# Optimization experiments

Hardware: AMD Instinct MI355X
Metric: run time of the kernel (lower is better)

Reference implementation:

```python
import jax, jax.numpy as jnp
import numpy as np

_DIR_INLIER = 0.9          # _HOUGHVOTING_DIRECTION_INLIER
_NUM_INLIER = 500          # _HOUGHVOTING_NUM_INLIER
_LABEL_THRESH = 500        # _LABEL2MASK_THRESHOL
NUM_CLASSES = 10
BS, H, W = 1, 240, 320


def setup_inputs() -> dict:
    key = jax.random.key(0)
    k_lab, k_cx, k_cy, k_nx, k_ny, k_nd = jax.random.split(key, 6)
    label = jax.random.randint(k_lab, (BS, H, W), 0, NUM_CLASSES + 1).astype(jnp.int32)
    xs = jnp.arange(W, dtype=jnp.float32)
    ys = jnp.arange(H, dtype=jnp.float32)
    xv, yv = jnp.meshgrid(xs, ys)  # [H, W] each
    # per-class ground-truth centers well inside the image so voting converges
    cxs = jax.random.uniform(k_cx, (NUM_CLASSES,), minval=40.0, maxval=W - 40.0)
    cys = jax.random.uniform(k_cy, (NUM_CLASSES,), minval=40.0, maxval=H - 40.0)
    dx = cxs[:, None, None] - xv[None]  # [C, H, W]
    dy = cys[:, None, None] - yv[None]
    nrm = jnp.sqrt(dx * dx + dy * dy) + 1e-6
    dirx = dx / nrm + 0.01 * jax.random.normal(k_nx, (NUM_CLASSES, H, W))
    diry = dy / nrm + 0.01 * jax.random.normal(k_ny, (NUM_CLASSES, H, W))
    depth = (1.0 + 0.3 * jnp.arange(NUM_CLASSES, dtype=jnp.float32))[:, None, None] \
        + 0.01 * jax.random.normal(k_nd, (NUM_CLASSES, H, W))
    cmap = jnp.stack([dirx, diry, depth], axis=1).reshape(3 * NUM_CLASSES, H, W)
    centermap = jnp.broadcast_to(cmap[None], (BS, 3 * NUM_CLASSES, H, W)).astype(jnp.float32)
    return {"label": label, "centermap": centermap}


def hough_voting(label, centermap, num_classes):
    bs, H_, W_ = label.shape
    xs = jnp.arange(W_, dtype=jnp.float32)
    ys = jnp.arange(H_, dtype=jnp.float32)
    xv, yv = jnp.meshgrid(xs, ys)            # [H, W]
    xsi = jnp.arange(W_, dtype=jnp.int32)
    all_centers, all_depths = [], []
    for b in range(bs):
        lab = label[b]
        row_c, row_d = [], []
        for cls in range(1, num_classes + 1):
            cmask = lab == cls                                    # [H, W]
            enough = cmask.sum() >= _LABEL_THRESH
            c3 = centermap[b, (cls - 1) * 3:(cls - 1) * 3 + 3]    # [3, H, W]
            slope = c3[1] / c3[0]                                  # dy/dx per pixel
            # every masked pixel votes along its line at every column x
            y_idx = jnp.round(yv[:, :, None] + slope[:, :, None] * (xs[None, None, :] - xv[:, :, None])).astype(jnp.int32)  # [H, W, W]
            valid = (y_idx >= 0) & (y_idx < H_) & cmask[:, :, None]
            bins = jnp.clip(y_idx, 0, H_ - 1) * W_ + xsi[None, None, :]
            hist = jnp.zeros(H_ * W_, jnp.float32).at[bins.ravel()].add(valid.ravel().astype(jnp.float32))
            cbin = jnp.argmax(hist)
            inlier_num = hist[cbin]
            cx = (cbin % W_).astype(jnp.float32)
            cy = (cbin // W_).astype(jnp.float32)
            # depth: mean of depth channel over direction-consistent class pixels
            disx = xv - cx
            disy = yv - cy
            dnrm = jnp.sqrt(disx * disx + disy * disy)
            dot = jnp.abs((disx / dnrm) * c3[0] + (disy / dnrm) * c3[1])  # nan at center -> compares False, as torch
            imask = (dot >= _DIR_INLIER) & cmask
            cnt = imask.sum().astype(jnp.float32)
            dsum = jnp.sum(jnp.where(imask, c3[2], 0.0))
            dmean = jnp.where(cnt > 0, dsum / jnp.maximum(cnt, 1.0), jnp.nan)
            trig = enough & (inlier_num > _NUM_INLIER)
            row_c.append(jnp.where(trig, jnp.stack([cx, cy]), jnp.zeros(2, jnp.float32)))
            row_d.append(jnp.where(trig, dmean, 0.0))
        all_centers.append(jnp.stack(row_c))
        all_depths.append(jnp.stack(row_d))
    return jnp.stack(all_centers), jnp.stack(all_depths)


def reference(label, centermap):
    return hough_voting(label, centermap, NUM_CLASSES)
```

## Files before the change

kernel.cpp:

```cpp
#include <hip/hip_runtime.h>
#include <stdint.h>

#define H 240
#define W 320
#define NPIX (H * W)
#define NCLS 10
#define TILE 16
#define HPAD 241
#define BIN_BITS 20
#define BIN_MASK 0xFFFFFu


__global__ void k_init(uint32_t* ws) {
    int i = threadIdx.x;
    if (i < 128) ws[i] = 0;
}

__global__ __launch_bounds__(256) void k_compact(const int* __restrict__ label,
                                                 const float* __restrict__ cm,
                                                 uint32_t* __restrict__ cls_cnt,
                                                 uint2* __restrict__ list) {
    __shared__ uint32_t lcnt[NCLS];
    __shared__ uint32_t lbase[NCLS];
    int p = blockIdx.x * 256 + threadIdx.x;
    if (threadIdx.x < NCLS) lcnt[threadIdx.x] = 0;
    __syncthreads();

    int l = label[p];
    bool match = (l >= 1 && l <= NCLS);
    int cls = l - 1;
    uint32_t li = 0;
    if (match) li = atomicAdd(&lcnt[cls], 1u);
    __syncthreads();

    if (threadIdx.x < NCLS) {
        uint32_t c = lcnt[threadIdx.x];
        lbase[threadIdx.x] = c ? atomicAdd(&cls_cnt[threadIdx.x], c) : 0u;
    }
    __syncthreads();

    if (match) {
        float dirx = cm[(cls * 3 + 0) * NPIX + p];
        float diry = cm[(cls * 3 + 1) * NPIX + p];
        float slope = diry / dirx;
        int y = p / W, x = p - y * W;
        uint2 e;
        e.x = (uint32_t)(x | (y << 16));
        e.y = __float_as_uint(slope);
        list[cls * NPIX + lbase[cls] + li] = e;
    }
}

__global__ __launch_bounds__(1024) void k_vote(const uint32_t* __restrict__ cls_cnt,
                                               const uint2* __restrict__ list,
                                               unsigned long long* __restrict__ best) {
    int cls = blockIdx.y;
    int x0 = blockIdx.x * TILE;
    __shared__ uint32_t hist[TILE * HPAD];
    __shared__ unsigned long long wred[16];
    int tid = threadIdx.x;
    for (int i = tid; i < TILE * HPAD; i += 1024) hist[i] = 0;
    __syncthreads();

    int n = (int)cls_cnt[cls];
    const uint2* lst = list + cls * NPIX;
    int wave = tid >> 6, lane = tid & 63;
    int g = lane >> 4, cit = lane & 15;
    float colf = (float)(x0 + cit);
    uint32_t* hcol = &hist[cit * HPAD];
    for (int i = wave * 4 + g; i < n; i += 64) {
        uint2 e = lst[i];
        float slope = __uint_as_float(e.y);
        float xf = (float)(e.x & 0xFFFFu);
        float yf = (float)(e.x >> 16);
        float r = rintf(yf + slope * (colf - xf));
        if (r >= 0.0f && r <= 239.0f) atomicAdd(&hcol[(int)r], 1u);
    }
    __syncthreads();

    unsigned long long k = 0;
    for (int i = tid; i < TILE * H; i += 1024) {
        int c = i / H, y = i - c * H;
        uint32_t v = hist[c * HPAD + y];
        uint32_t bin = (uint32_t)(y * W + x0 + c);
        unsigned long long key =
            ((unsigned long long)v << BIN_BITS) | (unsigned long long)(BIN_MASK - bin);
        if (key > k) k = key;
    }
#pragma unroll
    for (int off = 32; off > 0; off >>= 1) {
        unsigned long long o = __shfl_down(k, off);
        if (o > k) k = o;
    }
    if (lane == 0) wred[wave] = k;
    __syncthreads();
    if (tid == 0) {
        unsigned long long kk = wred[0];
#pragma unroll
        for (int w = 1; w < 16; ++w) if (wred[w] > kk) kk = wred[w];
        atomicMax(&best[cls], kk);
    }
}

__global__ __launch_bounds__(256) void k_inlier_final(
    const int* __restrict__ label, const float* __restrict__ cm,
    const uint32_t* __restrict__ cls_cnt,
    const unsigned long long* __restrict__ best,
    uint32_t* __restrict__ icnt, float* __restrict__ dsum,
    uint32_t* __restrict__ done, float* __restrict__ out) {
    __shared__ float scx[NCLS], scy[NCLS];
    __shared__ uint32_t scnt[NCLS];
    __shared__ float ssum[NCLS];
    __shared__ int slast;
    int tid = threadIdx.x;
    if (tid < NCLS) {
        unsigned long long key = best[tid];
        uint32_t bin = BIN_MASK - (uint32_t)(key & BIN_MASK);
        scx[tid] = (float)(bin % W);
        scy[tid] = (float)(bin / W);
        scnt[tid] = 0u;
        ssum[tid] = 0.0f;
    }
    __syncthreads();

    int p = blockIdx.x * 256 + tid;
    int l = label[p];
    if (l >= 1 && l <= NCLS) {
        int cls = l - 1;
        int y = p / W, x = p - y * W;
        float disx = (float)x - scx[cls];
        float disy = (float)y - scy[cls];
        float dn = sqrtf(disx * disx + disy * disy);
        if (dn > 0.0f) {
            float c0 = cm[(cls * 3 + 0) * NPIX + p];
            float c1 = cm[(cls * 3 + 1) * NPIX + p];
            float dot = fabsf((disx / dn) * c0 + (disy / dn) * c1);
            if (dot >= 0.9f) {
                atomicAdd(&scnt[cls], 1u);
                atomicAdd(&ssum[cls], cm[(cls * 3 + 2) * NPIX + p]);
            }
        }
    }
    __syncthreads();

    if (tid < NCLS) {
        if (scnt[tid]) atomicAdd(&icnt[tid], scnt[tid]);
        if (ssum[tid] != 0.0f) atomicAdd(&dsum[tid], ssum[tid]);
    }
    if (tid == 0) {
        __threadfence();
        uint32_t d = atomicAdd(done, 1u);
        slast = (d == (uint32_t)(gridDim.x - 1)) ? 1 : 0;
    }
    __syncthreads();

    if (slast && tid < NCLS) {
        uint32_t tc = atomicAdd(&icnt[tid], 0u);
        float td = atomicAdd(&dsum[tid], 0.0f);
        unsigned long long key = best[tid];
        uint32_t hv = (uint32_t)(key >> BIN_BITS);
        bool trig = (cls_cnt[tid] >= 500u) && (hv > 500u);
        float c = (float)tc;
        float dm = (c > 0.0f) ? (td / fmaxf(c, 1.0f)) : __builtin_nanf("");
        out[tid * 2 + 0] = trig ? scx[tid] : 0.0f;
        out[tid * 2 + 1] = trig ? scy[tid] : 0.0f;
        out[2 * NCLS + tid] = trig ? dm : 0.0f;
    }
}

extern "C" void kernel_launch(void* const* d_in, const int* in_sizes, int n_in,
                              void* d_out, int out_size, void* d_ws, size_t ws_size,
                              hipStream_t stream) {
    const int* label = (const int*)d_in[0];
    const float* cm = (const float*)d_in[1];
    float* out = (float*)d_out;
    char* ws = (char*)d_ws;

    uint32_t* cls_cnt = (uint32_t*)(ws + 0);
    unsigned long long* best = (unsigned long long*)(ws + 64);
    uint32_t* icnt = (uint32_t*)(ws + 192);
    float* dsum = (float*)(ws + 256);
    uint32_t* done = (uint32_t*)(ws + 320);
    uint2* list = (uint2*)(ws + 512);

    k_init<<<1, 128, 0, stream>>>((uint32_t*)ws);
    k_compact<<<NPIX / 256, 256, 0, stream>>>(label, cm, cls_cnt, list);
    k_vote<<<dim3(W / TILE, NCLS), 1024, 0, stream>>>(cls_cnt, list, best);
    k_inlier_final<<<NPIX / 256, 256, 0, stream>>>(label, cm, cls_cnt, best,
                                                   icnt, dsum, done, out);
}
```

Measured before the change: 114.6 us.

## Fuse init, compaction, voting and inlier passes into one cooperative kernel

Replaces four separate kernel launches with a single cooperative-groups kernel of 300 blocks of 256 threads, using grid-wide syncs between the phases. The voting phase now runs on 200 of the blocks with 256 threads each instead of 200 blocks of 1024 threads, so each block walks the class list in strides of 16 rather than 64. The goal is to remove launch and inter-kernel gaps. In exchange each voting block does four times more serial work, grid.sync has its own cost, and the rest of the grid sits idle during voting.

```diff
diff --git a/kernel.cpp b/kernel.cpp
--- a/kernel.cpp
+++ b/kernel.cpp
@@ -1,118 +1,115 @@
 #include <hip/hip_runtime.h>
+#include <hip/hip_cooperative_groups.h>
 #include <stdint.h>
+
+namespace cg = cooperative_groups;
 
 #define H 240
 #define W 320
 #define NPIX (H * W)
 #define NCLS 10
-#define TILE 16
+#define VT 16
+#define NTILE (W / VT)
 #define HPAD 241
 #define BIN_BITS 20
 #define BIN_MASK 0xFFFFFu
 
 
-__global__ void k_init(uint32_t* ws) {
-    int i = threadIdx.x;
-    if (i < 128) ws[i] = 0;
-}
+__global__ __launch_bounds__(256) void k_fused(
+    const int* __restrict__ label, const float* __restrict__ cm,
+    uint32_t* __restrict__ cls_cnt, unsigned long long* __restrict__ best,
+    uint32_t* __restrict__ icnt, float* __restrict__ dsum,
+    uint32_t* __restrict__ done, uint2* __restrict__ list,
+    float* __restrict__ out, uint32_t* __restrict__ wsbase) {
+    cg::grid_group grid = cg::this_grid();
+    __shared__ uint32_t sh[VT * HPAD];
+    __shared__ uint32_t lcnt[NCLS], lbase[NCLS];
+    __shared__ unsigned long long wred[4];
+    __shared__ float scx[NCLS], scy[NCLS], ssum[NCLS];
+    __shared__ uint32_t scnt[NCLS];
+    __shared__ int slast;
 
-__global__ __launch_bounds__(256) void k_compact(const int* __restrict__ label,
-                                                 const float* __restrict__ cm,
-                                                 uint32_t* __restrict__ cls_cnt,
-                                                 uint2* __restrict__ list) {
-    __shared__ uint32_t lcnt[NCLS];
-    __shared__ uint32_t lbase[NCLS];
-    int p = blockIdx.x * 256 + threadIdx.x;
-    if (threadIdx.x < NCLS) lcnt[threadIdx.x] = 0;
-    __syncthreads();
+    const int tid = threadIdx.x;
+    const int b = blockIdx.x;
+    const int p = b * 256 + tid;
 
-    int l = label[p];
-    bool match = (l >= 1 && l <= NCLS);
-    int cls = l - 1;
-    uint32_t li = 0;
-    if (match) li = atomicAdd(&lcnt[cls], 1u);
-    __syncthreads();
+    if (b == 0 && tid < 128) wsbase[tid] = 0;
+    grid.sync();
 
-    if (threadIdx.x < NCLS) {
-        uint32_t c = lcnt[threadIdx.x];
-        lbase[threadIdx.x] = c ? atomicAdd(&cls_cnt[threadIdx.x], c) : 0u;
+    {
+        if (tid < NCLS) lcnt[tid] = 0;
+        __syncthreads();
+        int l = label[p];
+        bool match = (l >= 1 && l <= NCLS);
+        int cls = l - 1;
+        uint32_t li = 0;
+        if (match) li = atomicAdd(&lcnt[cls], 1u);
+        __syncthreads();
+        if (tid < NCLS) {
+            uint32_t c = lcnt[tid];
+            lbase[tid] = c ? atomicAdd(&cls_cnt[tid], c) : 0u;
+        }
+        __syncthreads();
+        if (match) {
+            float dirx = cm[(cls * 3 + 0) * NPIX + p];
+            float diry = cm[(cls * 3 + 1) * NPIX + p];
+            float slope = diry / dirx;
+            int y = p / W, x = p - y * W;
+            uint2 e;
+            e.x = (uint32_t)(x | (y << 16));
+            e.y = __float_as_uint(slope);
+            list[cls * NPIX + lbase[cls] + li] = e;
+        }
     }
-    __syncthreads();
+    grid.sync();
 
-    if (match) {
-        float dirx = cm[(cls * 3 + 0) * NPIX + p];
-        float diry = cm[(cls * 3 + 1) * NPIX + p];
-        float slope = diry / dirx;
-        int y = p / W, x = p - y * W;
-        uint2 e;
-        e.x = (uint32_t)(x | (y << 16));
-        e.y = __float_as_uint(slope);
-        list[cls * NPIX + lbase[cls] + li] = e;
+    if (b < NTILE * NCLS) {
+        int cls = b / NTILE, tile = b - cls * NTILE;
+        int x0 = tile * VT;
+        for (int i = tid; i < VT * HPAD; i += 256) sh[i] = 0;
+        __syncthreads();
+        if (tid == 0) lcnt[0] = atomicAdd(&cls_cnt[cls], 0u);
+        __syncthreads();
+        int n = (int)lcnt[0];
+        const uint2* lst = list + cls * NPIX;
+        int wave = tid >> 6, lane = tid & 63;
+        int grp = lane >> 4, cit = lane & 15;
+        float colf = (float)(x0 + cit);
+        uint32_t* hcol = &sh[cit * HPAD];
+        for (int i = wave * 4 + grp; i < n; i += 16) {
+            uint2 e = lst[i];
+            float slope = __uint_as_float(e.y);
+            float xf = (float)(e.x & 0xFFFFu);
+            float yf = (float)(e.x >> 16);
+            float r = rintf(yf + slope * (colf - xf));
+            if (r >= 0.0f && r <= 239.0f) atomicAdd(&hcol[(int)r], 1u);
+        }
+        __syncthreads();
+        unsigned long long k = 0;
+        for (int i = tid; i < VT * H; i += 256) {
+            int c = i / H, y = i - c * H;
+            uint32_t v = sh[c * HPAD + y];
+            uint32_t bin = (uint32_t)(y * W + x0 + c);
+            unsigned long long key =
+                ((unsigned long long)v << BIN_BITS) | (unsigned long long)(BIN_MASK - bin);
+            if (key > k) k = key;
+        }
+#pragma unroll
+        for (int off = 32; off > 0; off >>= 1) {
+            unsigned long long o = __shfl_down(k, off);
+            if (o > k) k = o;
+        }
+        if (lane == 0) wred[wave] = k;
+        __syncthreads();
+        if (tid == 0) {
+            unsigned long long kk = wred[0];
+#pragma unroll
+            for (int w = 1; w < 4; ++w) if (wred[w] > kk) kk = wred[w];
+            atomicMax(&best[cls], kk);
+        }
     }
-}
+    grid.sync();
 
-__global__ __launch_bounds__(1024) void k_vote(const uint32_t* __restrict__ cls_cnt,
-                                               const uint2* __restrict__ list,
-                                               unsigned long long* __restrict__ best) {
-    int cls = blockIdx.y;
-    int x0 = blockIdx.x * TILE;
-    __shared__ uint32_t hist[TILE * HPAD];
-    __shared__ unsigned long long wred[16];
-    int tid = threadIdx.x;
-    for (int i = tid; i < TILE * HPAD; i += 1024) hist[i] = 0;
-    __syncthreads();
-
-    int n = (int)cls_cnt[cls];
-    const uint2* lst = list + cls * NPIX;
-    int wave = tid >> 6, lane = tid & 63;
-    int g = lane >> 4, cit = lane & 15;
-    float colf = (float)(x0 + cit);
-    uint32_t* hcol = &hist[cit * HPAD];
-    for (int i = wave * 4 + g; i < n; i += 64) {
-        uint2 e = lst[i];
-        float slope = __uint_as_float(e.y);
-        float xf = (float)(e.x & 0xFFFFu);
-        float yf = (float)(e.x >> 16);
-        float r = rintf(yf + slope * (colf - xf));
-        if (r >= 0.0f && r <= 239.0f) atomicAdd(&hcol[(int)r], 1u);
-    }
-    __syncthreads();
-
-    unsigned long long k = 0;
-    for (int i = tid; i < TILE * H; i += 1024) {
-        int c = i / H, y = i - c * H;
-        uint32_t v = hist[c * HPAD + y];
-        uint32_t bin = (uint32_t)(y * W + x0 + c);
-        unsigned long long key =
-            ((unsigned long long)v << BIN_BITS) | (unsigned long long)(BIN_MASK - bin);
-        if (key > k) k = key;
-    }
-#pragma unroll
-    for (int off = 32; off > 0; off >>= 1) {
-        unsigned long long o = __shfl_down(k, off);
-        if (o > k) k = o;
-    }
-    if (lane == 0) wred[wave] = k;
-    __syncthreads();
-    if (tid == 0) {
-        unsigned long long kk = wred[0];
-#pragma unroll
-        for (int w = 1; w < 16; ++w) if (wred[w] > kk) kk = wred[w];
-        atomicMax(&best[cls], kk);
-    }
-}
-
-__global__ __launch_bounds__(256) void k_inlier_final(
-    const int* __restrict__ label, const float* __restrict__ cm,
-    const uint32_t* __restrict__ cls_cnt,
-    const unsigned long long* __restrict__ best,
-    uint32_t* __restrict__ icnt, float* __restrict__ dsum,
-    uint32_t* __restrict__ done, float* __restrict__ out) {
-    __shared__ float scx[NCLS], scy[NCLS];
-    __shared__ uint32_t scnt[NCLS];
-    __shared__ float ssum[NCLS];
-    __shared__ int slast;
-    int tid = threadIdx.x;
     if (tid < NCLS) {
         unsigned long long key = best[tid];
         uint32_t bin = BIN_MASK - (uint32_t)(key & BIN_MASK);
@@ -123,7 +120,6 @@
     }
     __syncthreads();
 
-    int p = blockIdx.x * 256 + tid;
     int l = label[p];
     if (l >= 1 && l <= NCLS) {
         int cls = l - 1;
@@ -157,9 +153,10 @@
     if (slast && tid < NCLS) {
         uint32_t tc = atomicAdd(&icnt[tid], 0u);
         float td = atomicAdd(&dsum[tid], 0.0f);
+        uint32_t cc = atomicAdd(&cls_cnt[tid], 0u);
         unsigned long long key = best[tid];
         uint32_t hv = (uint32_t)(key >> BIN_BITS);
-        bool trig = (cls_cnt[tid] >= 500u) && (hv > 500u);
+        bool trig = (cc >= 500u) && (hv > 500u);
         float c = (float)tc;
         float dm = (c > 0.0f) ? (td / fmaxf(c, 1.0f)) : __builtin_nanf("");
         out[tid * 2 + 0] = trig ? scx[tid] : 0.0f;
@@ -182,10 +179,11 @@
     float* dsum = (float*)(ws + 256);
     uint32_t* done = (uint32_t*)(ws + 320);
     uint2* list = (uint2*)(ws + 512);
+    uint32_t* wsbase = (uint32_t*)ws;
 
-    k_init<<<1, 128, 0, stream>>>((uint32_t*)ws);
-    k_compact<<<NPIX / 256, 256, 0, stream>>>(label, cm, cls_cnt, list);
-    k_vote<<<dim3(W / TILE, NCLS), 1024, 0, stream>>>(cls_cnt, list, best);
-    k_inlier_final<<<NPIX / 256, 256, 0, stream>>>(label, cm, cls_cnt, best,
-                                                   icnt, dsum, done, out);
+    void* args[] = {(void*)&label, (void*)&cm,   (void*)&cls_cnt, (void*)&best,
+                    (void*)&icnt,  (void*)&dsum, (void*)&done,    (void*)&list,
+                    (void*)&out,   (void*)&wsbase};
+    hipLaunchCooperativeKernel((const void*)k_fused, dim3(NPIX / 256), dim3(256),
+                               args, 0, stream);
 }
```

Result: slower. 305.6 us (+166.8%).
